# Kernel tuning notes

Hardware: AMD Instinct MI355X
Metric: run time of the kernel (lower is better)

The kernel has to match this reference:

```python
import jax, jax.numpy as jnp
import numpy as np

B, T, C = 8, 2048, 1024
H, D = 16, 64  # n_heads, head_size; H*D == C


def setup_inputs() -> dict:
    key = jax.random.key(0)
    ks = jax.random.split(key, 6)
    s = 0.02
    x = jax.random.normal(ks[0], (B, T, C), dtype=jnp.float32)
    wq = jax.random.normal(ks[1], (H, C, D), dtype=jnp.float32) * s
    wk = jax.random.normal(ks[2], (H, C, D), dtype=jnp.float32) * s
    wv = jax.random.normal(ks[3], (H, C, D), dtype=jnp.float32) * s
    w_proj = jax.random.normal(ks[4], (H * D, C), dtype=jnp.float32) * s
    b_proj = jax.random.normal(ks[5], (C,), dtype=jnp.float32) * s
    return {"x": x, "wq": wq, "wk": wk, "wv": wv, "w_proj": w_proj, "b_proj": b_proj}


def reference(x, wq, wk, wv, w_proj, b_proj):
    Bq, Tq, Cq = x.shape
    # Batched per-head projections (original loops over heads with separate Linears)
    q = jnp.einsum('btc,hcd->bhtd', x, wq)
    k = jnp.einsum('btc,hcd->bhtd', x, wk)
    v = jnp.einsum('btc,hcd->bhtd', x, wv)
    # NOTE: source scales by C**-0.5 where C is the INPUT embed dim, not head_size
    wei = jnp.einsum('bhtd,bhsd->bhts', q, k) * (Cq ** -0.5)
    causal = jnp.tril(jnp.ones((Tq, Tq), dtype=bool))
    wei = jnp.where(causal, wei, jnp.float32(-jnp.inf))
    wei = jax.nn.softmax(wei, axis=-1)
    # dropout is identity in eval/reference mode
    out = jnp.einsum('bhts,bhsd->bhtd', wei, v)
    out = out.transpose(0, 2, 1, 3).reshape(Bq, Tq, H * D)  # concat over heads
    return out @ w_proj + b_proj
```

## Files before the change

kernel.cpp:

```cpp
#include <hip/hip_runtime.h>
#include <stdint.h>

#define DEV static __device__ __forceinline__

typedef __attribute__((ext_vector_type(8))) short bf16x8;
typedef __attribute__((ext_vector_type(4))) float f32x4;

constexpr int Bc = 8, Tc = 2048, Cc = 1024, Hc = 16, Dc = 64;

DEV ushort f2bf(float f) {
  union { float f; uint32_t u; } x{f};
  uint32_t r = (x.u + 0x7FFFu + ((x.u >> 16) & 1u)) >> 16;
  return (ushort)r;
}

DEV uint32_t cvt_pk_bf16(float a, float b) {
  uint32_t r;
  asm("v_cvt_pk_bf16_f32 %0, %1, %2" : "=v"(r) : "v"(a), "v"(b));
  return r;
}

DEV float max3f(float a, float b, float c) {
  float r;
  asm("v_max3_f32 %0, %1, %2, %3" : "=v"(r) : "v"(a), "v"(b), "v"(c));
  return r;
}

DEV void gload16(const ushort* g, ushort* l) {
  __builtin_amdgcn_global_load_lds(
      (const __attribute__((address_space(1))) unsigned int*)g,
      (__attribute__((address_space(3))) unsigned int*)l, 16, 0, 0);
}

DEV f32x4 mfma16(bf16x8 a, bf16x8 b, f32x4 c) {
  return __builtin_amdgcn_mfma_f32_16x16x32_bf16(a, b, c, 0, 0, 0);
}

union B8 { bf16x8 v; uint4 u; };

DEV void vm4() { asm volatile("s_waitcnt vmcnt(4)" ::: "memory"); }
DEV void vm0() { asm volatile("s_waitcnt vmcnt(0)" ::: "memory"); }
DEV void memfence() { asm volatile("" ::: "memory"); }
DEV void pbar() {
  __builtin_amdgcn_sched_barrier(0);
  __builtin_amdgcn_s_barrier();
  __builtin_amdgcn_sched_barrier(0);
}

__global__ __launch_bounds__(256) void k_conv_x(const float* __restrict__ x, ushort* __restrict__ xb) {
  int i = blockIdx.x * 256 + threadIdx.x;
  float4 v = ((const float4*)x)[i];
  ushort4 o = make_ushort4(f2bf(v.x), f2bf(v.y), f2bf(v.z), f2bf(v.w));
  ((ushort4*)xb)[i] = o;
}

__global__ __launch_bounds__(256) void k_conv_wqkv(const float* __restrict__ wq, const float* __restrict__ wk,
                                                   const float* __restrict__ wv, ushort* __restrict__ wt) {
  int i = blockIdx.x * 256 + threadIdx.x;
  int c = i & 1023;
  int n = i >> 10;
  int which = n >> 10;
  int rem = n & 1023;
  int h = rem >> 6, d = rem & 63;
  const float* src = which == 0 ? wq : (which == 1 ? wk : wv);
  float v = src[((size_t)h * 1024 + c) * 64 + d];
  if (which == 0) v *= 0.03125f * 1.44269504088896340736f;
  wt[i] = f2bf(v);
}

__global__ __launch_bounds__(256) void k_conv_wproj(const float* __restrict__ wp, ushort* __restrict__ wt) {
  int i = blockIdx.x * 256 + threadIdx.x;
  int n = i >> 10, k = i & 1023;
  wt[i] = f2bf(wp[(size_t)k * 1024 + n]);
}

DEV void gemm256_main(const ushort* __restrict__ A, const ushort* __restrict__ B,
                      int m0, int n0, int tid, ushort* ldsA, ushort* ldsB,
                      f32x4 (&acc)[8][4]) {
  const int lane = tid & 63;
  const int lr = lane & 15, lg = lane >> 4;
  const int wid = tid >> 6;
  const int wm = wid >> 2, wn = wid & 3;
  constexpr int NT = 16;

  auto stageA = [&](int q, int t) {
#pragma unroll
    for (int j = 0; j < 2; ++j) {
      int c = tid + q * 512 + j * 1024;
      int row = c >> 3;
      int col = 8 * ((c & 7) ^ (row & 7));
      gload16(&A[(size_t)(m0 + row) * 1024 + t * 64 + col], &ldsA[(t & 1) * 16384 + c * 8]);
    }
  };
  auto stageB = [&](int q, int t) {
#pragma unroll
    for (int j = 0; j < 2; ++j) {
      int c = q * 256 + (tid & 255) + ((tid >> 8) + 2 * j) * 512;
      int row = c >> 3;
      int col = 8 * ((c & 7) ^ (row & 7));
      gload16(&B[(size_t)(n0 + row) * 1024 + t * 64 + col], &ldsB[(t & 1) * 16384 + c * 8]);
    }
  };
  auto rdA = [&](bf16x8 (&af)[2][4], const ushort* bA, int mh) {
#pragma unroll
    for (int kc = 0; kc < 2; ++kc)
#pragma unroll
      for (int mf = 0; mf < 4; ++mf) {
        int row = wm * 128 + mh * 64 + mf * 16 + lr;
        af[kc][mf] = *(const bf16x8*)((const char*)bA + row * 128 + ((kc * 64 + lg * 16) ^ ((row & 7) << 4)));
      }
  };
  auto rdB = [&](bf16x8 (&bf)[2][2], const ushort* bB, int nh) {
#pragma unroll
    for (int kc = 0; kc < 2; ++kc)
#pragma unroll
      for (int nf = 0; nf < 2; ++nf) {
        int row = wn * 64 + nh * 32 + nf * 16 + lr;
        bf[kc][nf] = *(const bf16x8*)((const char*)bB + row * 128 + ((kc * 64 + lg * 16) ^ ((row & 7) << 4)));
      }
  };

  stageA(0, 0); stageB(0, 0);
  memfence();
  stageA(1, 0); stageB(1, 0);
  vm4();
  pbar();

  for (int t = 0; t < NT; ++t) {
    const ushort* bA = ldsA + (t & 1) * 16384;
    const ushort* bB = ldsB + (t & 1) * 16384;
    const bool pf = (t + 1) < NT;
    bf16x8 af[2][4], bf0[2][2], bf1[2][2];
    if (pf) { stageA(0, t + 1); stageB(0, t + 1); }
    rdA(af, bA, 0);
    rdB(bf0, bB, 0);
    __builtin_amdgcn_s_setprio(1);
#pragma unroll
    for (int kc = 0; kc < 2; ++kc)
#pragma unroll
      for (int mf = 0; mf < 4; ++mf)
#pragma unroll
        for (int nf = 0; nf < 2; ++nf)
          acc[mf][nf] = mfma16(af[kc][mf], bf0[kc][nf], acc[mf][nf]);
    __builtin_amdgcn_s_setprio(0);
    if (pf) vm4(); else vm0();
    pbar();
    if (pf) stageA(1, t + 1);
    rdB(bf1, bB, 1);
    __builtin_amdgcn_s_setprio(1);
#pragma unroll
    for (int kc = 0; kc < 2; ++kc)
#pragma unroll
      for (int mf = 0; mf < 4; ++mf)
#pragma unroll
        for (int nf = 0; nf < 2; ++nf)
          acc[mf][2 + nf] = mfma16(af[kc][mf], bf1[kc][nf], acc[mf][2 + nf]);
    __builtin_amdgcn_s_setprio(0);
    if (pf) stageB(1, t + 1);
    rdA(af, bA, 1);
    __builtin_amdgcn_s_setprio(1);
#pragma unroll
    for (int kc = 0; kc < 2; ++kc)
#pragma unroll
      for (int mf = 0; mf < 4; ++mf)
#pragma unroll
        for (int nf = 0; nf < 2; ++nf)
          acc[4 + mf][nf] = mfma16(af[kc][mf], bf0[kc][nf], acc[4 + mf][nf]);
    __builtin_amdgcn_s_setprio(0);
    __builtin_amdgcn_s_setprio(1);
#pragma unroll
    for (int kc = 0; kc < 2; ++kc)
#pragma unroll
      for (int mf = 0; mf < 4; ++mf)
#pragma unroll
        for (int nf = 0; nf < 2; ++nf)
          acc[4 + mf][2 + nf] = mfma16(af[kc][mf], bf1[kc][nf], acc[4 + mf][2 + nf]);
    __builtin_amdgcn_s_setprio(0);
    if (pf) vm4(); else vm0();
    pbar();
  }
}

__global__ __launch_bounds__(512, 2) void k_gemm_qkv(const ushort* __restrict__ xb, const ushort* __restrict__ wt,
                                                     ushort* __restrict__ qws, ushort* __restrict__ kws,
                                                     ushort* __restrict__ vws) {
  __shared__ __align__(16) ushort ldsA[2 * 16384];
  __shared__ __align__(16) ushort ldsB[2 * 16384];
  const int tid = threadIdx.x;
  const int orig = blockIdx.x;
  const int wgid = (orig & 7) * 96 + (orig >> 3);
  const int bn = wgid >> 6, bm = wgid & 63;
  const int m0 = bm * 256, n0 = bn * 256;
  f32x4 acc[8][4];
  f32x4 z = {0.f, 0.f, 0.f, 0.f};
#pragma unroll
  for (int i = 0; i < 8; ++i)
#pragma unroll
    for (int j = 0; j < 4; ++j) acc[i][j] = z;
  gemm256_main(xb, wt, m0, n0, tid, ldsA, ldsB, acc);
  const int lane = tid & 63, wid = tid >> 6;
  const int lr = lane & 15, lg = lane >> 4;
  const int wm = wid >> 2, wn = wid & 3;
#pragma unroll
  for (int a = 0; a < 8; ++a)
#pragma unroll
    for (int nf = 0; nf < 4; ++nf)
#pragma unroll
      for (int r = 0; r < 4; ++r) {
        int m = m0 + wm * 128 + (a >> 2) * 64 + (a & 3) * 16 + lg * 4 + r;
        int n = n0 + wn * 64 + nf * 16 + lr;
        int which = n >> 10, rem = n & 1023;
        int h = rem >> 6, d = rem & 63;
        int b = m >> 11, t = m & 2047;
        ushort* dst = which == 0 ? qws : (which == 1 ? kws : vws);
        dst[((size_t)(b * Hc + h) * Tc + t) * 64 + d] = f2bf(acc[a][nf][r]);
      }
}

__global__ __launch_bounds__(512, 2) void k_gemm_proj(const ushort* __restrict__ attb, const ushort* __restrict__ wt,
                                                      const float* __restrict__ bias, float* __restrict__ out) {
  __shared__ __align__(16) ushort ldsA[2 * 16384];
  __shared__ __align__(16) ushort ldsB[2 * 16384];
  const int tid = threadIdx.x;
  const int orig = blockIdx.x;
  const int wgid = (orig & 7) * 32 + (orig >> 3);
  const int bn = wgid >> 6, bm = wgid & 63;
  const int m0 = bm * 256, n0 = bn * 256;
  f32x4 acc[8][4];
  f32x4 z = {0.f, 0.f, 0.f, 0.f};
#pragma unroll
  for (int i = 0; i < 8; ++i)
#pragma unroll
    for (int j = 0; j < 4; ++j) acc[i][j] = z;
  gemm256_main(attb, wt, m0, n0, tid, ldsA, ldsB, acc);
  const int lane = tid & 63, wid = tid >> 6;
  const int lr = lane & 15, lg = lane >> 4;
  const int wm = wid >> 2, wn = wid & 3;
#pragma unroll
  for (int a = 0; a < 8; ++a)
#pragma unroll
    for (int nf = 0; nf < 4; ++nf)
#pragma unroll
      for (int r = 0; r < 4; ++r) {
        int m = m0 + wm * 128 + (a >> 2) * 64 + (a & 3) * 16 + lg * 4 + r;
        int n = n0 + wn * 64 + nf * 16 + lr;
        out[(size_t)m * 1024 + n] = acc[a][nf][r] + bias[n];
      }
}

__global__ __launch_bounds__(256) void k_vtrans(const ushort* __restrict__ v, ushort* __restrict__ vt) {
  __shared__ ushort lds[64][68];
  const int t0 = blockIdx.x * 64;
  const int bh = blockIdx.y;
  const int tid = threadIdx.x;
  const ushort* src = v + (size_t)bh * Tc * 64;
  ushort* dst = vt + (size_t)bh * 64 * Tc;
#pragma unroll
  for (int j = 0; j < 4; ++j) {
    int flat = j * 256 + tid;
    int row = flat >> 4, cg = flat & 15;
    ushort4 x = *(const ushort4*)&src[(size_t)(t0 + row) * 64 + cg * 4];
    lds[row][cg * 4 + 0] = x.x; lds[row][cg * 4 + 1] = x.y;
    lds[row][cg * 4 + 2] = x.z; lds[row][cg * 4 + 3] = x.w;
  }
  __syncthreads();
#pragma unroll
  for (int j = 0; j < 4; ++j) {
    int flat = j * 256 + tid;
    int d = flat >> 4, tg = flat & 15;
    ushort4 x = make_ushort4(lds[tg * 4 + 0][d], lds[tg * 4 + 1][d], lds[tg * 4 + 2][d], lds[tg * 4 + 3][d]);
    *(ushort4*)&dst[(size_t)d * Tc + t0 + tg * 4] = x;
  }
}

DEV int swzK(int row, int bcol) { return row * 128 + (bcol ^ ((row & 7) << 4)); }
DEV int swzV(int row, int bcol) { return row * 256 + (bcol ^ ((row & 7) << 4)); }

__global__ __launch_bounds__(256) void k_attn(const ushort* __restrict__ qws, const ushort* __restrict__ kws,
                                              const ushort* __restrict__ vtws, ushort* __restrict__ att) {
  const int id = blockIdx.x;
  const int xcd = id & 7, slot = id >> 3;
  const int bh = (xcd << 4) + (slot >> 3);
  const int qi = slot & 7;
  const int tid = threadIdx.x, lane = tid & 63, wid = tid >> 6;
  const int lr = lane & 15, lg = lane >> 4;

  __shared__ __align__(16) ushort lds_k[2 * 128 * 64];
  __shared__ __align__(16) ushort lds_v[2 * 64 * 128];

  const ushort* qbase = qws + (size_t)bh * Tc * 64;
  const ushort* kbase = kws + (size_t)bh * Tc * 64;
  const ushort* vtbase = vtws + (size_t)bh * 64 * Tc;
  const int b = bh >> 4, h = bh & 15;
  const f32x4 z = {0.f, 0.f, 0.f, 0.f};

  int rowK[4], colK[4], rowV[4], colV[4];
#pragma unroll
  for (int r = 0; r < 4; ++r) {
    int c = r * 256 + tid;
    rowK[r] = c >> 3; colK[r] = 8 * ((c & 7) ^ (rowK[r] & 7));
    rowV[r] = c >> 4; colV[r] = 8 * ((c & 15) ^ (rowV[r] & 7));
  }

  B8 onesf;
  {
    uint32_t pp = lr == 0 ? 0x3F803F80u : 0u;
    onesf.u = make_uint4(pp, pp, pp, pp);
  }

  for (int pass = 0; pass < 2; ++pass) {
    const int qb = pass == 0 ? qi : 15 - qi;
    const int q0 = qb * 128;
    const int ntiles = qb + 1;
    const int qrow = q0 + wid * 32;
    const int qgmax = qrow + 31;

    bf16x8 qa[2][2];
#pragma unroll
    for (int qf = 0; qf < 2; ++qf)
#pragma unroll
      for (int kc = 0; kc < 2; ++kc)
        qa[qf][kc] = *(const bf16x8*)&qbase[(size_t)(qrow + qf * 16 + lr) * 64 + kc * 32 + lg * 8];

    f32x4 o[2][4];
    f32x4 lac[2];
    float m_[2];
#pragma unroll
    for (int qf = 0; qf < 2; ++qf) {
#pragma unroll
      for (int df = 0; df < 4; ++df) o[qf][df] = z;
      lac[qf] = z;
      m_[qf] = -1e30f;
    }

    __syncthreads();

#pragma unroll
    for (int r = 0; r < 4; ++r) {
      gload16(&kbase[(size_t)rowK[r] * 64 + colK[r]], &lds_k[(r * 256 + tid) * 8]);
      gload16(&vtbase[(size_t)rowV[r] * Tc + colV[r]], &lds_v[(r * 256 + tid) * 8]);
    }

    for (int it = 0; it < ntiles; ++it) {
      __syncthreads();
      const ushort* ldsK = lds_k + (it & 1) * 8192;
      const ushort* ldsV = lds_v + (it & 1) * 8192;
      if (it + 1 < ntiles) {
        const int s0n = (it + 1) * 128;
        ushort* dK = lds_k + ((it + 1) & 1) * 8192;
        ushort* dV = lds_v + ((it + 1) & 1) * 8192;
#pragma unroll
        for (int r = 0; r < 4; ++r) {
          gload16(&kbase[(size_t)(s0n + rowK[r]) * 64 + colK[r]], &dK[(r * 256 + tid) * 8]);
          gload16(&vtbase[(size_t)rowV[r] * Tc + s0n + colV[r]], &dV[(r * 256 + tid) * 8]);
        }
      }

      const int s0 = it * 128;
      const bool diag = (it == ntiles - 1);
      const int nlive = diag ? 2 * wid + 2 : 8;

      f32x4 s[8][2];
#pragma unroll
      for (int sf = 0; sf < 8; ++sf)
#pragma unroll
        for (int qf = 0; qf < 2; ++qf) s[sf][qf] = z;
#pragma unroll
      for (int kc = 0; kc < 2; ++kc) {
        bf16x8 kf[8];
#pragma unroll
        for (int sf = 0; sf < 8; ++sf)
          if (sf < nlive)
            kf[sf] = *(const bf16x8*)((const char*)ldsK + swzK(sf * 16 + lr, kc * 64 + lg * 16));
        __builtin_amdgcn_s_setprio(1);
#pragma unroll
        for (int sf = 0; sf < 8; ++sf)
          if (sf < nlive)
#pragma unroll
            for (int qf = 0; qf < 2; ++qf)
              s[sf][qf] = mfma16(kf[sf], qa[qf][kc], s[sf][qf]);
        __builtin_amdgcn_s_setprio(0);
      }

      if (diag) {
#pragma unroll
        for (int sf = 0; sf < 8; ++sf)
#pragma unroll
          for (int qf = 0; qf < 2; ++qf)
#pragma unroll
            for (int r = 0; r < 4; ++r) {
              int sg = s0 + sf * 16 + lg * 4 + r;
              int qg = qrow + qf * 16 + lr;
              if (sg > qg) s[sf][qf][r] = -1e30f;
            }
      }

      float sc[2];
      bool defer[2];
#pragma unroll
      for (int qf = 0; qf < 2; ++qf) {
        float rs[8];
#pragma unroll
        for (int sf = 0; sf < 8; ++sf)
          rs[sf] = fmaxf(max3f(s[sf][qf][0], s[sf][qf][1], s[sf][qf][2]), s[sf][qf][3]);
        float t = max3f(max3f(rs[0], rs[1], rs[2]), max3f(rs[3], rs[4], rs[5]), fmaxf(rs[6], rs[7]));
        t = fmaxf(t, __shfl_xor(t, 16));
        t = fmaxf(t, __shfl_xor(t, 32));
        defer[qf] = __all(t <= m_[qf] + 11.54f) != 0;
        float mnew = defer[qf] ? m_[qf] : fmaxf(m_[qf], t);
        sc[qf] = defer[qf] ? 1.f : exp2f(m_[qf] - mnew);
        m_[qf] = mnew;
#pragma unroll
        for (int sf = 0; sf < 8; ++sf)
#pragma unroll
          for (int r = 0; r < 4; ++r)
            s[sf][qf][r] = exp2f(s[sf][qf][r] - mnew);
      }
#pragma unroll
      for (int qf = 0; qf < 2; ++qf)
        if (!defer[qf]) {
#pragma unroll
          for (int r = 0; r < 4; ++r) {
            float scR = __shfl(sc[qf], ((lane >> 4) << 2) + r);
#pragma unroll
            for (int df = 0; df < 4; ++df) o[qf][df][r] *= scR;
            lac[qf][r] *= scR;
          }
        }

      uint32_t pk_[8][2][2];
#pragma unroll
      for (int sf = 0; sf < 8; ++sf)
#pragma unroll
        for (int qf = 0; qf < 2; ++qf) {
          pk_[sf][qf][0] = cvt_pk_bf16(s[sf][qf][0], s[sf][qf][1]);
          pk_[sf][qf][1] = cvt_pk_bf16(s[sf][qf][2], s[sf][qf][3]);
        }

#pragma unroll
      for (int kc = 0; kc < 4; ++kc) {
        B8 vf[4];
#pragma unroll
        for (int df = 0; df < 4; ++df) {
          uint2 lo = *(const uint2*)((const char*)ldsV + swzV(df * 16 + lr, kc * 64 + lg * 8));
          uint2 hi = *(const uint2*)((const char*)ldsV + swzV(df * 16 + lr, kc * 64 + 32 + lg * 8));
          vf[df].u = make_uint4(lo.x, lo.y, hi.x, hi.y);
        }
        B8 pf[2];
#pragma unroll
        for (int qf = 0; qf < 2; ++qf)
          pf[qf].u = make_uint4(pk_[2 * kc][qf][0], pk_[2 * kc][qf][1],
                                pk_[2 * kc + 1][qf][0], pk_[2 * kc + 1][qf][1]);
        __builtin_amdgcn_s_setprio(1);
#pragma unroll
        for (int qf = 0; qf < 2; ++qf) {
#pragma unroll
          for (int df = 0; df < 4; ++df)
            o[qf][df] = mfma16(pf[qf].v, vf[df].v, o[qf][df]);
          lac[qf] = mfma16(pf[qf].v, onesf.v, lac[qf]);
        }
        __builtin_amdgcn_s_setprio(0);
      }
    }

#pragma unroll
    for (int qf = 0; qf < 2; ++qf)
#pragma unroll
      for (int r = 0; r < 4; ++r) {
        float lR = __shfl(lac[qf][r], lg << 4);
        float inv = 1.f / lR;
        int qg = qrow + qf * 16 + lg * 4 + r;
#pragma unroll
        for (int df = 0; df < 4; ++df) {
          int d = df * 16 + lr;
          att[(size_t)(b * Tc + qg) * 1024 + h * 64 + d] = f2bf(o[qf][df][r] * inv);
        }
      }
  }
}

extern "C" void kernel_launch(void* const* d_in, const int* in_sizes, int n_in,
                              void* d_out, int out_size, void* d_ws, size_t ws_size,
                              hipStream_t stream) {
  const float* x  = (const float*)d_in[0];
  const float* wq = (const float*)d_in[1];
  const float* wk = (const float*)d_in[2];
  const float* wv = (const float*)d_in[3];
  const float* wp = (const float*)d_in[4];
  const float* bp = (const float*)d_in[5];
  float* out = (float*)d_out;

  char* ws = (char*)d_ws;
  size_t off = 0;
  auto alloc = [&](size_t bytes) { char* p = ws + off; off += (bytes + 255) & ~255ull; return p; };
  ushort* xb   = (ushort*)alloc(16384ull * 1024 * 2);
  ushort* wqkv = (ushort*)alloc(3072ull * 1024 * 2);
  ushort* wpt  = (ushort*)alloc(1024ull * 1024 * 2);
  ushort* qws  = (ushort*)alloc(16384ull * 1024 * 2);
  ushort* kws  = (ushort*)alloc(16384ull * 1024 * 2);
  ushort* vws  = (ushort*)alloc(16384ull * 1024 * 2);
  ushort* vtws = (ushort*)alloc(16384ull * 1024 * 2);
  ushort* attb = xb;

  k_conv_x<<<16384, 256, 0, stream>>>(x, xb);
  k_conv_wqkv<<<12288, 256, 0, stream>>>(wq, wk, wv, wqkv);
  k_conv_wproj<<<4096, 256, 0, stream>>>(wp, wpt);
  k_gemm_qkv<<<768, 512, 0, stream>>>(xb, wqkv, qws, kws, vws);
  k_vtrans<<<dim3(32, 128), 256, 0, stream>>>(vws, vtws);
  k_attn<<<1024, 256, 0, stream>>>(qws, kws, vtws, attb);
  k_gemm_proj<<<256, 512, 0, stream>>>(attb, wpt, bp, out);
}
```

Baseline: 545.1 us.

## Fuse V transpose into QKV GEMM epilogue and widen attention blocks to 256 queries

The QKV GEMM epilogue now writes V directly in transposed (d-major) layout using 4-element vector stores, removing the separate transpose kernel and its intermediate buffer round trip. The attention kernel moves to 512-thread blocks covering 256 query rows per pass, with 8 waves sharing each K/V tile load. Causal skipping and masking become per-wave: a wave skips tiles entirely above its rows and masks any tile that overlaps its diagonal. This halves the grid and raises in-block reuse of K/V, at the cost of waves idling on the diagonal tiles and strided vt stores from the GEMM.

```diff
diff --git a/kernel.cpp b/kernel.cpp
--- a/kernel.cpp
+++ b/kernel.cpp
@@ -183,7 +183,7 @@
 
 __global__ __launch_bounds__(512, 2) void k_gemm_qkv(const ushort* __restrict__ xb, const ushort* __restrict__ wt,
                                                      ushort* __restrict__ qws, ushort* __restrict__ kws,
-                                                     ushort* __restrict__ vws) {
+                                                     ushort* __restrict__ vtws) {
   __shared__ __align__(16) ushort ldsA[2 * 16384];
   __shared__ __align__(16) ushort ldsB[2 * 16384];
   const int tid = threadIdx.x;
@@ -204,17 +204,23 @@
 #pragma unroll
   for (int a = 0; a < 8; ++a)
 #pragma unroll
-    for (int nf = 0; nf < 4; ++nf)
-#pragma unroll
-      for (int r = 0; r < 4; ++r) {
-        int m = m0 + wm * 128 + (a >> 2) * 64 + (a & 3) * 16 + lg * 4 + r;
-        int n = n0 + wn * 64 + nf * 16 + lr;
-        int which = n >> 10, rem = n & 1023;
-        int h = rem >> 6, d = rem & 63;
-        int b = m >> 11, t = m & 2047;
-        ushort* dst = which == 0 ? qws : (which == 1 ? kws : vws);
-        dst[((size_t)(b * Hc + h) * Tc + t) * 64 + d] = f2bf(acc[a][nf][r]);
-      }
+    for (int nf = 0; nf < 4; ++nf) {
+      const int mbase = m0 + wm * 128 + (a >> 2) * 64 + (a & 3) * 16 + lg * 4;
+      const int n = n0 + wn * 64 + nf * 16 + lr;
+      const int which = n >> 10, rem = n & 1023;
+      const int h = rem >> 6, d = rem & 63;
+      const int b = mbase >> 11, t = mbase & 2047;
+      if (which == 2) {
+        ushort4 vv = make_ushort4(f2bf(acc[a][nf][0]), f2bf(acc[a][nf][1]),
+                                  f2bf(acc[a][nf][2]), f2bf(acc[a][nf][3]));
+        *(ushort4*)&vtws[((size_t)(b * Hc + h) * 64 + d) * Tc + t] = vv;
+      } else {
+        ushort* dst = which == 0 ? qws : kws;
+#pragma unroll
+        for (int r = 0; r < 4; ++r)
+          dst[((size_t)(b * Hc + h) * Tc + (t + r)) * 64 + d] = f2bf(acc[a][nf][r]);
+      }
+    }
 }
 
 __global__ __launch_bounds__(512, 2) void k_gemm_proj(const ushort* __restrict__ attb, const ushort* __restrict__ wt,
@@ -248,40 +254,15 @@
       }
 }
 
-__global__ __launch_bounds__(256) void k_vtrans(const ushort* __restrict__ v, ushort* __restrict__ vt) {
-  __shared__ ushort lds[64][68];
-  const int t0 = blockIdx.x * 64;
-  const int bh = blockIdx.y;
-  const int tid = threadIdx.x;
-  const ushort* src = v + (size_t)bh * Tc * 64;
-  ushort* dst = vt + (size_t)bh * 64 * Tc;
-#pragma unroll
-  for (int j = 0; j < 4; ++j) {
-    int flat = j * 256 + tid;
-    int row = flat >> 4, cg = flat & 15;
-    ushort4 x = *(const ushort4*)&src[(size_t)(t0 + row) * 64 + cg * 4];
-    lds[row][cg * 4 + 0] = x.x; lds[row][cg * 4 + 1] = x.y;
-    lds[row][cg * 4 + 2] = x.z; lds[row][cg * 4 + 3] = x.w;
-  }
-  __syncthreads();
-#pragma unroll
-  for (int j = 0; j < 4; ++j) {
-    int flat = j * 256 + tid;
-    int d = flat >> 4, tg = flat & 15;
-    ushort4 x = make_ushort4(lds[tg * 4 + 0][d], lds[tg * 4 + 1][d], lds[tg * 4 + 2][d], lds[tg * 4 + 3][d]);
-    *(ushort4*)&dst[(size_t)d * Tc + t0 + tg * 4] = x;
-  }
-}
-
 DEV int swzK(int row, int bcol) { return row * 128 + (bcol ^ ((row & 7) << 4)); }
 DEV int swzV(int row, int bcol) { return row * 256 + (bcol ^ ((row & 7) << 4)); }
 
-__global__ __launch_bounds__(256) void k_attn(const ushort* __restrict__ qws, const ushort* __restrict__ kws,
+__global__ __launch_bounds__(512) void k_attn(const ushort* __restrict__ qws, const ushort* __restrict__ kws,
                                               const ushort* __restrict__ vtws, ushort* __restrict__ att) {
   const int id = blockIdx.x;
   const int xcd = id & 7, slot = id >> 3;
-  const int bh = (xcd << 4) + (slot >> 3);
-  const int qi = slot & 7;
+  const int bh = (xcd << 4) + (slot >> 2);
+  const int pr = slot & 3;
   const int tid = threadIdx.x, lane = tid & 63, wid = tid >> 6;
   const int lr = lane & 15, lg = lane >> 4;
 
@@ -294,12 +275,12 @@
   const int b = bh >> 4, h = bh & 15;
   const f32x4 z = {0.f, 0.f, 0.f, 0.f};
 
-  int rowK[4], colK[4], rowV[4], colV[4];
-#pragma unroll
-  for (int r = 0; r < 4; ++r) {
-    int c = r * 256 + tid;
-    rowK[r] = c >> 3; colK[r] = 8 * ((c & 7) ^ (rowK[r] & 7));
-    rowV[r] = c >> 4; colV[r] = 8 * ((c & 15) ^ (rowV[r] & 7));
+  int rowK[2], colK[2], rowV[2], colV[2];
+#pragma unroll
+  for (int r = 0; r < 2; ++r) {
+    int c = r * 512 + tid;
+    rowK[r] = c >> 3;  colK[r] = 8 * ((c & 7) ^ (rowK[r] & 7));
+    rowV[r] = c >> 4;  colV[r] = 8 * ((c & 15) ^ (rowV[r] & 7));
   }
 
   B8 onesf;
@@ -309,9 +290,9 @@
   }
 
   for (int pass = 0; pass < 2; ++pass) {
-    const int qb = pass == 0 ? qi : 15 - qi;
-    const int q0 = qb * 128;
-    const int ntiles = qb + 1;
+    const int qb = pass == 0 ? pr : 7 - pr;
+    const int q0 = qb * 256;
+    const int ntiles = 2 * qb + 2;
     const int qrow = q0 + wid * 32;
     const int qgmax = qrow + 31;
 
@@ -336,9 +317,9 @@
     __syncthreads();
 
 #pragma unroll
-    for (int r = 0; r < 4; ++r) {
-      gload16(&kbase[(size_t)rowK[r] * 64 + colK[r]], &lds_k[(r * 256 + tid) * 8]);
-      gload16(&vtbase[(size_t)rowV[r] * Tc + colV[r]], &lds_v[(r * 256 + tid) * 8]);
+    for (int r = 0; r < 2; ++r) {
+      gload16(&kbase[(size_t)rowK[r] * 64 + colK[r]], &lds_k[(r * 512 + tid) * 8]);
+      gload16(&vtbase[(size_t)rowV[r] * Tc + colV[r]], &lds_v[(r * 512 + tid) * 8]);
     }
 
     for (int it = 0; it < ntiles; ++it) {
@@ -350,15 +331,16 @@
         ushort* dK = lds_k + ((it + 1) & 1) * 8192;
         ushort* dV = lds_v + ((it + 1) & 1) * 8192;
 #pragma unroll
-        for (int r = 0; r < 4; ++r) {
-          gload16(&kbase[(size_t)(s0n + rowK[r]) * 64 + colK[r]], &dK[(r * 256 + tid) * 8]);
-          gload16(&vtbase[(size_t)rowV[r] * Tc + s0n + colV[r]], &dV[(r * 256 + tid) * 8]);
+        for (int r = 0; r < 2; ++r) {
+          gload16(&kbase[(size_t)(s0n + rowK[r]) * 64 + colK[r]], &dK[(r * 512 + tid) * 8]);
+          gload16(&vtbase[(size_t)rowV[r] * Tc + s0n + colV[r]], &dV[(r * 512 + tid) * 8]);
         }
       }
 
       const int s0 = it * 128;
-      const bool diag = (it == ntiles - 1);
-      const int nlive = diag ? 2 * wid + 2 : 8;
+      if (s0 > qgmax) continue;
+      const int nlive = min(8, ((qgmax - s0) >> 4) + 1);
+      const bool maskNeeded = (s0 + 127 > qrow);
 
       f32x4 s[8][2];
 #pragma unroll
@@ -382,7 +364,7 @@
         __builtin_amdgcn_s_setprio(0);
       }
 
-      if (diag) {
+      if (maskNeeded) {
 #pragma unroll
         for (int sf = 0; sf < 8; ++sf)
 #pragma unroll
@@ -498,15 +480,13 @@
   ushort* wpt  = (ushort*)alloc(1024ull * 1024 * 2);
   ushort* qws  = (ushort*)alloc(16384ull * 1024 * 2);
   ushort* kws  = (ushort*)alloc(16384ull * 1024 * 2);
-  ushort* vws  = (ushort*)alloc(16384ull * 1024 * 2);
   ushort* vtws = (ushort*)alloc(16384ull * 1024 * 2);
   ushort* attb = xb;
 
   k_conv_x<<<16384, 256, 0, stream>>>(x, xb);
   k_conv_wqkv<<<12288, 256, 0, stream>>>(wq, wk, wv, wqkv);
   k_conv_wproj<<<4096, 256, 0, stream>>>(wp, wpt);
-  k_gemm_qkv<<<768, 512, 0, stream>>>(xb, wqkv, qws, kws, vws);
-  k_vtrans<<<dim3(32, 128), 256, 0, stream>>>(vws, vtws);
-  k_attn<<<1024, 256, 0, stream>>>(qws, kws, vtws, attb);
+  k_gemm_qkv<<<768, 512, 0, stream>>>(xb, wqkv, qws, kws, vtws);
+  k_attn<<<512, 512, 0, stream>>>(qws, kws, vtws, attb);
   k_gemm_proj<<<256, 512, 0, stream>>>(attb, wpt, bp, out);
 }
```

Measured after the change: 484.5 us. -11.1%, faster.
